# Optimization experiments

Hardware: AMD Instinct MI355X
Metric: run time of the kernel (lower is better)

The kernel has to match this reference:

```python
import jax, jax.numpy as jnp
import numpy as np

N, E = 50000, 800000
IN, HID, H, C = 128, 64, 4, 2
NEG_SLOPE = 0.2


def _gat_layer(h, src, dst, W, al, ar, b, out_dim, residual, resW=None, act='elu'):
    # h: [N, in]; W: [H*out, in]; al/ar: [H, out]; b: [H*out]
    n = h.shape[0]
    feat = (h @ W.T).reshape(n, H, out_dim)            # [N, H, out]
    el = jnp.einsum('nho,ho->nh', feat, al)            # [N, H]
    er = jnp.einsum('nho,ho->nh', feat, ar)            # [N, H]
    e = jax.nn.leaky_relu(el[src] + er[dst], NEG_SLOPE)  # [E, H]
    # segment softmax over incoming edges of each dst node
    emax = jax.ops.segment_max(e, dst, num_segments=n)
    ee = jnp.exp(e - emax[dst])
    denom = jax.ops.segment_sum(ee, dst, num_segments=n)
    alpha = ee / denom[dst]                             # [E, H]
    msg = feat[src] * alpha[:, :, None]                 # [E, H, out]
    rst = jax.ops.segment_sum(msg, dst, num_segments=n)  # [N, H, out]
    if residual == 'id':
        rst = rst + h.reshape(n, H, out_dim)
    elif residual == 'fc':
        rst = rst + (h @ resW.T).reshape(n, H, out_dim)
    rst = rst + b.reshape(1, H, out_dim)
    if act == 'elu':
        rst = jax.nn.elu(rst)
    else:  # softmax over last dim (F.softmax)
        rst = jax.nn.softmax(rst, axis=-1)
    return rst


def setup_inputs() -> dict:
    key = jax.random.key(0)
    ks = jax.random.split(key, 24)
    x = jax.random.normal(ks[0], (N, IN), dtype=jnp.float32)
    src = jax.random.randint(ks[1], (E,), 0, N)
    dst = jax.random.randint(ks[2], (E,), 0, N)
    s = 0.1
    d = {'x': x, 'src': src, 'dst': dst}
    # layer 1: IN -> (H, HID), no residual
    d['W1'] = jax.random.normal(ks[3], (H * HID, IN), dtype=jnp.float32) * s
    d['al1'] = jax.random.normal(ks[4], (H, HID), dtype=jnp.float32) * s
    d['ar1'] = jax.random.normal(ks[5], (H, HID), dtype=jnp.float32) * s
    d['b1'] = jnp.zeros((H * HID,), dtype=jnp.float32)
    # layers 2,3: H*HID -> (H, HID), identity residual
    d['W2'] = jax.random.normal(ks[6], (H * HID, H * HID), dtype=jnp.float32) * s
    d['al2'] = jax.random.normal(ks[7], (H, HID), dtype=jnp.float32) * s
    d['ar2'] = jax.random.normal(ks[8], (H, HID), dtype=jnp.float32) * s
    d['b2'] = jnp.zeros((H * HID,), dtype=jnp.float32)
    d['W3'] = jax.random.normal(ks[9], (H * HID, H * HID), dtype=jnp.float32) * s
    d['al3'] = jax.random.normal(ks[10], (H, HID), dtype=jnp.float32) * s
    d['ar3'] = jax.random.normal(ks[11], (H, HID), dtype=jnp.float32) * s
    d['b3'] = jnp.zeros((H * HID,), dtype=jnp.float32)
    # layer 4: H*HID -> (H, C), linear residual, softmax activation, mean over heads
    d['W4'] = jax.random.normal(ks[12], (H * C, H * HID), dtype=jnp.float32) * s
    d['al4'] = jax.random.normal(ks[13], (H, C), dtype=jnp.float32) * s
    d['ar4'] = jax.random.normal(ks[14], (H, C), dtype=jnp.float32) * s
    d['b4'] = jnp.zeros((H * C,), dtype=jnp.float32)
    d['resW4'] = jax.random.normal(ks[15], (H * C, H * HID), dtype=jnp.float32) * s
    return d


def reference(x, src, dst, W1, al1, ar1, b1, W2, al2, ar2, b2, W3, al3, ar3, b3, W4, al4, ar4, b4, resW4):
    h = _gat_layer(x, src, dst, W1, al1, ar1, b1, HID, 'none', act='elu').reshape(N, H * HID)
    h = _gat_layer(h, src, dst, W2, al2, ar2, b2, HID, 'id', act='elu').reshape(N, H * HID)
    h = _gat_layer(h, src, dst, W3, al3, ar3, b3, HID, 'id', act='elu').reshape(N, H * HID)
    h = _gat_layer(h, src, dst, W4, al4, ar4, b4, C, 'fc', resW=resW4, act='softmax')
    return h.mean(axis=1)  # [N, C]
```

## Files before the change

### kernel.cpp

```cpp
#include <hip/hip_runtime.h>
#include <hip/hip_bf16.h>
#include <math.h>


#define LEAKY_SLOPE 0.2f

typedef __bf16 bf16x8_t __attribute__((ext_vector_type(8)));
typedef float f32x4_t __attribute__((ext_vector_type(4)));

__device__ __forceinline__ float leaky(float x) { return x > 0.f ? x : LEAKY_SLOPE * x; }
__device__ __forceinline__ float eluf(float x)  { return x > 0.f ? x : expm1f(x); }
__device__ __forceinline__ float bflo(unsigned u) { return __uint_as_float(u << 16); }
__device__ __forceinline__ float bfhi(unsigned u) { return __uint_as_float(u & 0xffff0000u); }

__device__ __forceinline__ int rli(int v, int l) { return __builtin_amdgcn_readlane(v, l); }
__device__ __forceinline__ float rlf(float v, int l) {
  return __uint_as_float((unsigned)__builtin_amdgcn_readlane((int)__float_as_uint(v), l));
}
template <int CTRL>
__device__ __forceinline__ float dpp_add(float x) {
  int t = __builtin_amdgcn_update_dpp(0, (int)__float_as_uint(x), CTRL, 0xf, 0xf, false);
  return x + __uint_as_float((unsigned)t);
}
__device__ __forceinline__ float wsum_dpp(float x) {
  x = dpp_add<0x111>(x);
  x = dpp_add<0x112>(x);
  x = dpp_add<0x114>(x);
  x = dpp_add<0x118>(x);
  x = dpp_add<0x142>(x);
  x = dpp_add<0x143>(x);
  return rlf(x, 63);
}
__device__ __forceinline__ float wmax(float v) {
#pragma unroll
  for (int o = 32; o; o >>= 1) v = fmaxf(v, __shfl_xor(v, o));
  return v;
}
__device__ __forceinline__ float wsum_sh(float v) {
#pragma unroll
  for (int o = 32; o; o >>= 1) v += __shfl_xor(v, o);
  return v;
}

__global__ void hist_k(const int* __restrict__ dst, int* __restrict__ deg, int e) {
  int i = blockIdx.x * 256 + threadIdx.x;
  if (i < e) atomicAdd(&deg[dst[i]], 1);
}

__global__ __launch_bounds__(1024) void scan1_k(const int* __restrict__ deg,
                                                int* __restrict__ rowp,
                                                int* __restrict__ bsum, int n) {
  __shared__ int sd[1024];
  int tid = threadIdx.x;
  int i = blockIdx.x * 1024 + tid;
  int v = (i < n) ? deg[i] : 0;
  int x = v;
  sd[tid] = x;
  __syncthreads();
  for (int off = 1; off < 1024; off <<= 1) {
    int t = (tid >= off) ? sd[tid - off] : 0;
    __syncthreads();
    x += t;
    sd[tid] = x;
    __syncthreads();
  }
  if (i < n) rowp[i] = x - v;
  if (tid == 1023) bsum[blockIdx.x] = x;
}

__global__ __launch_bounds__(64) void scan2_k(int* __restrict__ bsum, int nb) {
  int lane = threadIdx.x;
  if (nb <= 64) {
    int v = (lane < nb) ? bsum[lane] : 0;
    int x = v;
#pragma unroll
    for (int off = 1; off < 64; off <<= 1) {
      int t = __shfl_up(x, off);
      if (lane >= off) x += t;
    }
    if (lane < nb) bsum[lane] = x - v;
    if (lane == 63) bsum[nb] = x;
  } else if (lane == 0) {
    int run = 0;
    for (int i = 0; i < nb; ++i) { int t = bsum[i]; bsum[i] = run; run += t; }
    bsum[nb] = run;
  }
}

__global__ void scan3_k(const int* __restrict__ bsum, int* __restrict__ rowp, int n, int nb) {
  int i = blockIdx.x * 256 + threadIdx.x;
  if (i < n) rowp[i] += bsum[i >> 10];
  if (i == n) rowp[n] = bsum[nb];
}

__global__ void scatter_k(const int* __restrict__ src, const int* __restrict__ dst,
                          const int* __restrict__ rowp, int* __restrict__ cur,
                          int* __restrict__ csrc, int e) {
  int i = blockIdx.x * 256 + threadIdx.x;
  if (i < e) {
    int d = dst[i];
    int p = atomicAdd(&cur[d], 1);
    csrc[rowp[d] + p] = src[i];
  }
}

__global__ void cvt_k(const float* __restrict__ a, __hip_bfloat16* __restrict__ b, int cnt) {
  int i = blockIdx.x * 256 + threadIdx.x;
  if (i < cnt) b[i] = __float2bfloat16(a[i]);
}

__global__ void cvtw_k(const float* __restrict__ W1, const float* __restrict__ W2,
                       const float* __restrict__ W3, const float* __restrict__ W4,
                       const float* __restrict__ rW4, __hip_bfloat16* __restrict__ W1b,
                       __hip_bfloat16* __restrict__ W2b, __hip_bfloat16* __restrict__ W3b,
                       __hip_bfloat16* __restrict__ Wcatb) {
  int i = blockIdx.x * 256 + threadIdx.x;
  if (i < 32768) W1b[i] = __float2bfloat16(W1[i]);
  else if (i < 98304)  { int j = i - 32768;  W2b[j] = __float2bfloat16(W2[j]); }
  else if (i < 163840) { int j = i - 98304;  W3b[j] = __float2bfloat16(W3[j]); }
  else if (i < 165888) { int j = i - 163840; Wcatb[j] = __float2bfloat16(W4[j]); }
  else if (i < 167936) { int j = i - 165888; Wcatb[2048 + j] = __float2bfloat16(rW4[j]); }
}

__global__ void wa_all_k(const float* __restrict__ W1, const float* __restrict__ al1,
                         const float* __restrict__ ar1, float* __restrict__ Wal1,
                         float* __restrict__ War1, const float* __restrict__ W2,
                         const float* __restrict__ al2, const float* __restrict__ ar2,
                         float* __restrict__ Wal2, float* __restrict__ War2,
                         const float* __restrict__ W3, const float* __restrict__ al3,
                         const float* __restrict__ ar3, float* __restrict__ Wal3,
                         float* __restrict__ War3) {
  int i = blockIdx.x * 256 + threadIdx.x;
  const float *W, *al, *ar;
  float *Wal, *War;
  int K, idx;
  if (i < 512)       { W = W1; al = al1; ar = ar1; Wal = Wal1; War = War1; K = 128; idx = i; }
  else if (i < 1536) { W = W2; al = al2; ar = ar2; Wal = Wal2; War = War2; K = 256; idx = i - 512; }
  else if (i < 2560) { W = W3; al = al3; ar = ar3; Wal = Wal3; War = War3; K = 256; idx = i - 1536; }
  else return;
  int hh = idx / K, col = idx - hh * K;
  float sl = 0.f, sr = 0.f;
  const float* wp = W + (size_t)(hh * 64) * K + col;
#pragma unroll 4
  for (int o = 0; o < 64; ++o) {
    float wv = wp[(size_t)o * K];
    sl = fmaf(al[hh * 64 + o], wv, sl);
    sr = fmaf(ar[hh * 64 + o], wv, sr);
  }
  Wal[idx] = sl;
  War[idx] = sr;
}

__global__ __launch_bounds__(256) void elproj_k(const float* __restrict__ x,
                                                const float* __restrict__ Wal,
                                                const float* __restrict__ War,
                                                float* __restrict__ el,
                                                float* __restrict__ er, int n) {
  int node = blockIdx.x * 4 + (threadIdx.x >> 6);
  int lane = threadIdx.x & 63;
  if (node >= n) return;
  float2 xv = *(const float2*)(x + (size_t)node * 128 + lane * 2);
#pragma unroll
  for (int hh = 0; hh < 4; ++hh) {
    float sl = xv.x * Wal[hh * 128 + 2 * lane] + xv.y * Wal[hh * 128 + 2 * lane + 1];
    float sr = xv.x * War[hh * 128 + 2 * lane] + xv.y * War[hh * 128 + 2 * lane + 1];
    sl = wsum_dpp(sl);
    sr = wsum_dpp(sr);
    if (lane == 0) {
      el[node * 4 + hh] = sl;
      er[node * 4 + hh] = sr;
    }
  }
}

template <int K>
__global__ __launch_bounds__(256) void gemm_mfma(const __hip_bfloat16* __restrict__ A,
                                                 const __hip_bfloat16* __restrict__ B,
                                                 __hip_bfloat16* __restrict__ featb, int n) {
  __shared__ __bf16 As[128 * 40];
  __shared__ __bf16 Bs[128 * 40];
  const int tid = threadIdx.x;
  const int lane = tid & 63, w = tid >> 6;
  const int tm = lane & 15, tq = lane >> 4;
  const int wm = (w & 1) * 64, wn = (w >> 1) * 64;
  const int r0 = blockIdx.x * 128, c0 = blockIdx.y * 128;
  const int srow = tid >> 1, sko = (tid & 1) * 16;

  f32x4_t acc[4][4];
#pragma unroll
  for (int i = 0; i < 4; ++i)
#pragma unroll
    for (int j = 0; j < 4; ++j) acc[i][j] = 0.f;

  for (int kk = 0; kk < K; kk += 32) {
    uint4 av0 = {0, 0, 0, 0}, av1 = {0, 0, 0, 0};
    int arw = r0 + srow;
    if (arw < n) {
      const uint4* p = (const uint4*)(A + (size_t)arw * K + kk + sko);
      av0 = p[0];
      av1 = p[1];
    }
    const uint4* q = (const uint4*)(B + (size_t)(c0 + srow) * K + kk + sko);
    uint4 bv0 = q[0], bv1 = q[1];
    __syncthreads();
    *(uint4*)&As[srow * 40 + sko] = av0;
    *(uint4*)&As[srow * 40 + sko + 8] = av1;
    *(uint4*)&Bs[srow * 40 + sko] = bv0;
    *(uint4*)&Bs[srow * 40 + sko + 8] = bv1;
    __syncthreads();
    bf16x8_t af[4], bfr[4];
#pragma unroll
    for (int i = 0; i < 4; ++i) af[i] = *(const bf16x8_t*)&As[(wm + i * 16 + tm) * 40 + tq * 8];
#pragma unroll
    for (int j = 0; j < 4; ++j) bfr[j] = *(const bf16x8_t*)&Bs[(wn + j * 16 + tm) * 40 + tq * 8];
#pragma unroll
    for (int i = 0; i < 4; ++i)
#pragma unroll
      for (int j = 0; j < 4; ++j)
        acc[i][j] = __builtin_amdgcn_mfma_f32_16x16x32_bf16(af[i], bfr[j], acc[i][j], 0, 0, 0);
  }

#pragma unroll
  for (int i = 0; i < 4; ++i) {
#pragma unroll
    for (int j = 0; j < 4; ++j) {
      int col = c0 + wn + j * 16 + tm;
      int hh = col >> 6, oo = col & 63;
#pragma unroll
      for (int rr = 0; rr < 4; ++rr) {
        int row = r0 + wm + i * 16 + tq * 4 + rr;
        if (row < n) featb[(size_t)row * 256 + oo * 4 + hh] = __float2bfloat16(acc[i][j][rr]);
      }
    }
  }
}

template <int RES, int NEXT>
__global__ __launch_bounds__(256) void agg64_k(const __hip_bfloat16* __restrict__ featb,
                                               const float* __restrict__ el,
                                               const float* __restrict__ er,
                                               const int* __restrict__ rowp,
                                               const int* __restrict__ csrc,
                                               const __hip_bfloat16* __restrict__ hinb,
                                               const float* __restrict__ bias,
                                               __hip_bfloat16* __restrict__ houtb,
                                               const float* __restrict__ Waln,
                                               const float* __restrict__ Warn,
                                               float* __restrict__ eln,
                                               float* __restrict__ ern, int n) {
  int node = blockIdx.x * 4 + (threadIdx.x >> 6);
  int lane = threadIdx.x & 63;
  if (node >= n) return;
  int s0 = rowp[node], s1 = rowp[node + 1];
  int deg = s1 - s0;
  float4 erv = *(const float4*)(er + (size_t)node * 4);
  float a0 = 0, a1 = 0, a2 = 0, a3 = 0;
  float i0 = 1.f, i1 = 1.f, i2 = 1.f, i3 = 1.f;

  if (deg <= 64) {
    int sown = 0;
    float x0 = 0.f, x1 = 0.f, x2 = 0.f, x3 = 0.f;
    if (lane < deg) {
      sown = csrc[s0 + lane];
      float4 e = *(const float4*)(el + (size_t)sown * 4);
      x0 = __expf(leaky(e.x + erv.x));
      x1 = __expf(leaky(e.y + erv.y));
      x2 = __expf(leaky(e.z + erv.z));
      x3 = __expf(leaky(e.w + erv.w));
    }
    float d0 = wsum_dpp(x0), d1 = wsum_dpp(x1), d2 = wsum_dpp(x2), d3 = wsum_dpp(x3);
    i0 = d0 > 0.f ? 1.f / d0 : 0.f;
    i1 = d1 > 0.f ? 1.f / d1 : 0.f;
    i2 = d2 > 0.f ? 1.f / d2 : 0.f;
    i3 = d3 > 0.f ? 1.f / d3 : 0.f;

    int k = 0;
    for (; k + 4 <= deg; k += 4) {
      int sk0 = rli(sown, k + 0), sk1 = rli(sown, k + 1);
      int sk2 = rli(sown, k + 2), sk3 = rli(sown, k + 3);
      uint2 u0 = ((const uint2*)(featb + ((size_t)sk0 << 8)))[lane];
      uint2 u1 = ((const uint2*)(featb + ((size_t)sk1 << 8)))[lane];
      uint2 u2 = ((const uint2*)(featb + ((size_t)sk2 << 8)))[lane];
      uint2 u3 = ((const uint2*)(featb + ((size_t)sk3 << 8)))[lane];
      float w00 = rlf(x0, k + 0), w10 = rlf(x1, k + 0), w20 = rlf(x2, k + 0), w30 = rlf(x3, k + 0);
      float w01 = rlf(x0, k + 1), w11 = rlf(x1, k + 1), w21 = rlf(x2, k + 1), w31 = rlf(x3, k + 1);
      float w02 = rlf(x0, k + 2), w12 = rlf(x1, k + 2), w22 = rlf(x2, k + 2), w32 = rlf(x3, k + 2);
      float w03 = rlf(x0, k + 3), w13 = rlf(x1, k + 3), w23 = rlf(x2, k + 3), w33 = rlf(x3, k + 3);
      a0 = fmaf(w00, bflo(u0.x), a0); a1 = fmaf(w10, bfhi(u0.x), a1);
      a2 = fmaf(w20, bflo(u0.y), a2); a3 = fmaf(w30, bfhi(u0.y), a3);
      a0 = fmaf(w01, bflo(u1.x), a0); a1 = fmaf(w11, bfhi(u1.x), a1);
      a2 = fmaf(w21, bflo(u1.y), a2); a3 = fmaf(w31, bfhi(u1.y), a3);
      a0 = fmaf(w02, bflo(u2.x), a0); a1 = fmaf(w12, bfhi(u2.x), a1);
      a2 = fmaf(w22, bflo(u2.y), a2); a3 = fmaf(w32, bfhi(u2.y), a3);
      a0 = fmaf(w03, bflo(u3.x), a0); a1 = fmaf(w13, bfhi(u3.x), a1);
      a2 = fmaf(w23, bflo(u3.y), a2); a3 = fmaf(w33, bfhi(u3.y), a3);
    }
    for (; k < deg; ++k) {
      int sk = rli(sown, k);
      float w0k = rlf(x0, k), w1k = rlf(x1, k), w2k = rlf(x2, k), w3k = rlf(x3, k);
      uint2 u = ((const uint2*)(featb + ((size_t)sk << 8)))[lane];
      a0 = fmaf(w0k, bflo(u.x), a0);
      a1 = fmaf(w1k, bfhi(u.x), a1);
      a2 = fmaf(w2k, bflo(u.y), a2);
      a3 = fmaf(w3k, bfhi(u.y), a3);
    }
  } else {
    float m0 = -INFINITY, m1 = -INFINITY, m2 = -INFINITY, m3 = -INFINITY;
    for (int k = s0 + lane; k < s1; k += 64) {
      int s = csrc[k];
      float4 e = *(const float4*)(el + (size_t)s * 4);
      m0 = fmaxf(m0, leaky(e.x + erv.x));
      m1 = fmaxf(m1, leaky(e.y + erv.y));
      m2 = fmaxf(m2, leaky(e.z + erv.z));
      m3 = fmaxf(m3, leaky(e.w + erv.w));
    }
    m0 = wmax(m0); m1 = wmax(m1); m2 = wmax(m2); m3 = wmax(m3);
    float d0 = 0, d1 = 0, d2 = 0, d3 = 0;
    for (int k = s0 + lane; k < s1; k += 64) {
      int s = csrc[k];
      float4 e = *(const float4*)(el + (size_t)s * 4);
      d0 += __expf(leaky(e.x + erv.x) - m0);
      d1 += __expf(leaky(e.y + erv.y) - m1);
      d2 += __expf(leaky(e.z + erv.z) - m2);
      d3 += __expf(leaky(e.w + erv.w) - m3);
    }
    d0 = wsum_sh(d0); d1 = wsum_sh(d1); d2 = wsum_sh(d2); d3 = wsum_sh(d3);
    float j0 = d0 > 0.f ? 1.f / d0 : 0.f;
    float j1 = d1 > 0.f ? 1.f / d1 : 0.f;
    float j2 = d2 > 0.f ? 1.f / d2 : 0.f;
    float j3 = d3 > 0.f ? 1.f / d3 : 0.f;
    for (int k = s0; k < s1; ++k) {
      int s = csrc[k];
      float4 e = *(const float4*)(el + (size_t)s * 4);
      float w0 = __expf(leaky(e.x + erv.x) - m0) * j0;
      float w1 = __expf(leaky(e.y + erv.y) - m1) * j1;
      float w2 = __expf(leaky(e.z + erv.z) - m2) * j2;
      float w3 = __expf(leaky(e.w + erv.w) - m3) * j3;
      uint2 u = ((const uint2*)(featb + ((size_t)s << 8)))[lane];
      a0 = fmaf(w0, bflo(u.x), a0);
      a1 = fmaf(w1, bfhi(u.x), a1);
      a2 = fmaf(w2, bflo(u.y), a2);
      a3 = fmaf(w3, bfhi(u.y), a3);
    }
  }

  size_t base = (size_t)node * 256;
  float v0 = a0 * i0 + bias[lane];
  float v1 = a1 * i1 + bias[64 + lane];
  float v2 = a2 * i2 + bias[128 + lane];
  float v3 = a3 * i3 + bias[192 + lane];
  if (RES) {
    v0 += __bfloat162float(hinb[base + lane]);
    v1 += __bfloat162float(hinb[base + 64 + lane]);
    v2 += __bfloat162float(hinb[base + 128 + lane]);
    v3 += __bfloat162float(hinb[base + 192 + lane]);
  }
  float o0 = eluf(v0), o1 = eluf(v1), o2 = eluf(v2), o3 = eluf(v3);
  houtb[base + lane]       = __float2bfloat16(o0);
  houtb[base + 64 + lane]  = __float2bfloat16(o1);
  houtb[base + 128 + lane] = __float2bfloat16(o2);
  houtb[base + 192 + lane] = __float2bfloat16(o3);
  if (NEXT) {
#pragma unroll
    for (int hh = 0; hh < 4; ++hh) {
      float sl = o0 * Waln[hh * 256 + lane] + o1 * Waln[hh * 256 + 64 + lane] +
                 o2 * Waln[hh * 256 + 128 + lane] + o3 * Waln[hh * 256 + 192 + lane];
      float sr = o0 * Warn[hh * 256 + lane] + o1 * Warn[hh * 256 + 64 + lane] +
                 o2 * Warn[hh * 256 + 128 + lane] + o3 * Warn[hh * 256 + 192 + lane];
      sl = wsum_dpp(sl);
      sr = wsum_dpp(sr);
      if (lane == 0) {
        eln[node * 4 + hh] = sl;
        ern[node * 4 + hh] = sr;
      }
    }
  }
}

__global__ __launch_bounds__(256) void l4mfma_k(const __hip_bfloat16* __restrict__ hb,
                                                const __hip_bfloat16* __restrict__ Wcat,
                                                float* __restrict__ feat4,
                                                float* __restrict__ res4, int n) {
  int wid = blockIdx.x * 4 + (threadIdx.x >> 6);
  int n16 = (n + 15) >> 4;
  if (wid >= n16) return;
  int lane = threadIdx.x & 63;
  int tm = lane & 15, tq = lane >> 4;
  int row = wid * 16 + tm;
  int rowc = row < n ? row : n - 1;
  const __hip_bfloat16* ap = hb + (size_t)rowc * 256 + tq * 8;
  const __hip_bfloat16* bp = Wcat + (size_t)tm * 256 + tq * 8;
  f32x4_t acc = {0.f, 0.f, 0.f, 0.f};
#pragma unroll
  for (int k = 0; k < 8; ++k) {
    bf16x8_t af = *(const bf16x8_t*)(ap + k * 32);
    bf16x8_t bf = *(const bf16x8_t*)(bp + k * 32);
    acc = __builtin_amdgcn_mfma_f32_16x16x32_bf16(af, bf, acc, 0, 0, 0);
  }
  float* dstp = (tm < 8) ? feat4 : res4;
  int cc = tm & 7;
#pragma unroll
  for (int r = 0; r < 4; ++r) {
    int node = wid * 16 + tq * 4 + r;
    if (node < n) dstp[(size_t)node * 8 + cc] = acc[r];
  }
}

__global__ void el4er4_k(const float* __restrict__ feat4, const float* __restrict__ al4,
                         const float* __restrict__ ar4, float* __restrict__ el4,
                         float* __restrict__ er4, int n) {
  int i = blockIdx.x * 256 + threadIdx.x;
  if (i >= n) return;
  float4 f0 = ((const float4*)(feat4 + (size_t)i * 8))[0];
  float4 f1 = ((const float4*)(feat4 + (size_t)i * 8))[1];
  float4 lv, rv;
  lv.x = f0.x * al4[0] + f0.y * al4[1];
  lv.y = f0.z * al4[2] + f0.w * al4[3];
  lv.z = f1.x * al4[4] + f1.y * al4[5];
  lv.w = f1.z * al4[6] + f1.w * al4[7];
  rv.x = f0.x * ar4[0] + f0.y * ar4[1];
  rv.y = f0.z * ar4[2] + f0.w * ar4[3];
  rv.z = f1.x * ar4[4] + f1.y * ar4[5];
  rv.w = f1.z * ar4[6] + f1.w * ar4[7];
  *(float4*)(el4 + (size_t)i * 4) = lv;
  *(float4*)(er4 + (size_t)i * 4) = rv;
}

__global__ __launch_bounds__(256) void agg4_k(const float* __restrict__ feat4,
                                              const float* __restrict__ el4,
                                              const float* __restrict__ er4,
                                              const int* __restrict__ rowp,
                                              const int* __restrict__ csrc,
                                              const float* __restrict__ res4,
                                              const float* __restrict__ b4,
                                              float* __restrict__ out, int n) {
  int node = blockIdx.x * 4 + (threadIdx.x >> 6);
  int lane = threadIdx.x & 63;
  if (node >= n) return;
  int s0 = rowp[node], s1 = rowp[node + 1];
  int deg = s1 - s0;
  float4 erv = *(const float4*)(er4 + (size_t)node * 4);
  float acc = 0.f;
  float scale = 1.f;
  int p = lane & 7, hh = p >> 1;

  if (deg <= 64) {
    int sown = 0;
    float x0 = 0.f, x1 = 0.f, x2 = 0.f, x3 = 0.f;
    if (lane < deg) {
      sown = csrc[s0 + lane];
      float4 e = *(const float4*)(el4 + (size_t)sown * 4);
      x0 = __expf(leaky(e.x + erv.x));
      x1 = __expf(leaky(e.y + erv.y));
      x2 = __expf(leaky(e.z + erv.z));
      x3 = __expf(leaky(e.w + erv.w));
    }
    float d0 = wsum_dpp(x0), d1 = wsum_dpp(x1), d2 = wsum_dpp(x2), d3 = wsum_dpp(x3);
    float i0 = d0 > 0.f ? 1.f / d0 : 0.f;
    float i1 = d1 > 0.f ? 1.f / d1 : 0.f;
    float i2 = d2 > 0.f ? 1.f / d2 : 0.f;
    float i3 = d3 > 0.f ? 1.f / d3 : 0.f;
    scale = (hh == 0) ? i0 : (hh == 1) ? i1 : (hh == 2) ? i2 : i3;
    int g = lane >> 3;
    int nt = (deg + 7) >> 3;
    for (int t = 0; t < nt; ++t) {
      int k = g + t * 8;
      bool ok = k < deg;
      int kk = k & 63;
      int sk = __shfl(sown, kk);
      float x0k = __shfl(x0, kk), x1k = __shfl(x1, kk);
      float x2k = __shfl(x2, kk), x3k = __shfl(x3, kk);
      float wk = (hh == 0) ? x0k : (hh == 1) ? x1k : (hh == 2) ? x2k : x3k;
      if (ok) acc = fmaf(wk, feat4[(size_t)sk * 8 + p], acc);
    }
    acc += __shfl_xor(acc, 8);
    acc += __shfl_xor(acc, 16);
    acc += __shfl_xor(acc, 32);
  } else {
    float m0 = -INFINITY, m1 = -INFINITY, m2 = -INFINITY, m3 = -INFINITY;
    for (int k = s0 + lane; k < s1; k += 64) {
      int s = csrc[k];
      float4 e = *(const float4*)(el4 + (size_t)s * 4);
      m0 = fmaxf(m0, leaky(e.x + erv.x));
      m1 = fmaxf(m1, leaky(e.y + erv.y));
      m2 = fmaxf(m2, leaky(e.z + erv.z));
      m3 = fmaxf(m3, leaky(e.w + erv.w));
    }
    m0 = wmax(m0); m1 = wmax(m1); m2 = wmax(m2); m3 = wmax(m3);
    float d0 = 0, d1 = 0, d2 = 0, d3 = 0;
    for (int k = s0 + lane; k < s1; k += 64) {
      int s = csrc[k];
      float4 e = *(const float4*)(el4 + (size_t)s * 4);
      d0 += __expf(leaky(e.x + erv.x) - m0);
      d1 += __expf(leaky(e.y + erv.y) - m1);
      d2 += __expf(leaky(e.z + erv.z) - m2);
      d3 += __expf(leaky(e.w + erv.w) - m3);
    }
    d0 = wsum_sh(d0); d1 = wsum_sh(d1); d2 = wsum_sh(d2); d3 = wsum_sh(d3);
    float i0 = d0 > 0.f ? 1.f / d0 : 0.f;
    float i1 = d1 > 0.f ? 1.f / d1 : 0.f;
    float i2 = d2 > 0.f ? 1.f / d2 : 0.f;
    float i3 = d3 > 0.f ? 1.f / d3 : 0.f;
    for (int k = s0; k < s1; ++k) {
      int s = csrc[k];
      float4 e = *(const float4*)(el4 + (size_t)s * 4);
      float w0 = __expf(leaky(e.x + erv.x) - m0) * i0;
      float w1 = __expf(leaky(e.y + erv.y) - m1) * i1;
      float w2 = __expf(leaky(e.z + erv.z) - m2) * i2;
      float w3 = __expf(leaky(e.w + erv.w) - m3) * i3;
      float wk = (hh == 0) ? w0 : (hh == 1) ? w1 : (hh == 2) ? w2 : w3;
      if (lane < 8) acc = fmaf(wk, feat4[(size_t)s * 8 + p], acc);
    }
  }

  float v = 0.f;
  if (lane < 8) v = acc * scale + res4[(size_t)node * 8 + lane] + b4[lane];
  float pv = __shfl_xor(v, 1);
  float mx = fmaxf(v, pv);
  float ex = __expf(v - mx);
  float sm = ex + __shfl_xor(ex, 1);
  float pr = ex / sm;
  float t = pr + __shfl_xor(pr, 2);
  t += __shfl_xor(t, 4);
  if (lane < 2) out[(size_t)node * 2 + lane] = t * 0.25f;
}

extern "C" void kernel_launch(void* const* d_in, const int* in_sizes, int n_in,
                              void* d_out, int out_size, void* d_ws, size_t ws_size,
                              hipStream_t stream) {
  const float* x   = (const float*)d_in[0];
  const int* src   = (const int*)d_in[1];
  const int* dst   = (const int*)d_in[2];
  const float* W1  = (const float*)d_in[3];
  const float* al1 = (const float*)d_in[4];
  const float* ar1 = (const float*)d_in[5];
  const float* b1  = (const float*)d_in[6];
  const float* W2  = (const float*)d_in[7];
  const float* al2 = (const float*)d_in[8];
  const float* ar2 = (const float*)d_in[9];
  const float* b2  = (const float*)d_in[10];
  const float* W3  = (const float*)d_in[11];
  const float* al3 = (const float*)d_in[12];
  const float* ar3 = (const float*)d_in[13];
  const float* b3  = (const float*)d_in[14];
  const float* W4  = (const float*)d_in[15];
  const float* al4 = (const float*)d_in[16];
  const float* ar4 = (const float*)d_in[17];
  const float* b4  = (const float*)d_in[18];
  const float* rW4 = (const float*)d_in[19];
  float* out = (float*)d_out;

  const int n = in_sizes[0] / 128;
  const int e = in_sizes[1];

  char* ws = (char*)d_ws;
  auto alloc = [&](size_t bytes) -> char* {
    char* p = ws;
    ws += (bytes + 255) & ~(size_t)255;
    return p;
  };
  __hip_bfloat16* featb = (__hip_bfloat16*)alloc((size_t)n * 256 * 2);
  __hip_bfloat16* h1b   = (__hip_bfloat16*)alloc((size_t)n * 256 * 2);
  __hip_bfloat16* h2b   = (__hip_bfloat16*)alloc((size_t)n * 256 * 2);
  __hip_bfloat16* h3b   = (__hip_bfloat16*)alloc((size_t)n * 256 * 2);
  __hip_bfloat16* xb    = (__hip_bfloat16*)alloc((size_t)n * 128 * 2);
  __hip_bfloat16* W1b   = (__hip_bfloat16*)alloc((size_t)256 * 128 * 2);
  __hip_bfloat16* W2b   = (__hip_bfloat16*)alloc((size_t)256 * 256 * 2);
  __hip_bfloat16* W3b   = (__hip_bfloat16*)alloc((size_t)256 * 256 * 2);
  __hip_bfloat16* Wcatb = (__hip_bfloat16*)alloc((size_t)16 * 256 * 2);
  float* Wal1 = (float*)alloc((size_t)4 * 128 * 4);
  float* War1 = (float*)alloc((size_t)4 * 128 * 4);
  float* Wal2 = (float*)alloc((size_t)4 * 256 * 4);
  float* War2 = (float*)alloc((size_t)4 * 256 * 4);
  float* Wal3 = (float*)alloc((size_t)4 * 256 * 4);
  float* War3 = (float*)alloc((size_t)4 * 256 * 4);
  float* elA   = (float*)alloc((size_t)n * 4 * 4);
  float* erA   = (float*)alloc((size_t)n * 4 * 4);
  float* elB   = (float*)alloc((size_t)n * 4 * 4);
  float* erB   = (float*)alloc((size_t)n * 4 * 4);
  float* feat4 = (float*)alloc((size_t)n * 8 * 4);
  float* res4  = (float*)alloc((size_t)n * 8 * 4);
  float* el4   = (float*)alloc((size_t)n * 4 * 4);
  float* er4   = (float*)alloc((size_t)n * 4 * 4);
  int* deg     = (int*)alloc((size_t)n * 4);
  int* cur     = (int*)alloc((size_t)n * 4);
  int* rowp    = (int*)alloc((size_t)(n + 1) * 4);
  int* csrc    = (int*)alloc((size_t)e * 4);
  int nb_scan  = (n + 1023) / 1024;
  int* bsum    = (int*)alloc((size_t)(nb_scan + 1) * 4);

  (void)hipMemsetAsync(deg, 0, (size_t)n * 4, stream);
  (void)hipMemsetAsync(cur, 0, (size_t)n * 4, stream);
  hist_k<<<(e + 255) / 256, 256, 0, stream>>>(dst, deg, e);
  scan1_k<<<nb_scan, 1024, 0, stream>>>(deg, rowp, bsum, n);
  scan2_k<<<1, 64, 0, stream>>>(bsum, nb_scan);
  scan3_k<<<(n + 256) / 256, 256, 0, stream>>>(bsum, rowp, n, nb_scan);
  scatter_k<<<(e + 255) / 256, 256, 0, stream>>>(src, dst, rowp, cur, csrc, e);

  cvt_k<<<(n * 128 + 255) / 256, 256, 0, stream>>>(x, xb, n * 128);
  cvtw_k<<<(167936 + 255) / 256, 256, 0, stream>>>(W1, W2, W3, W4, rW4, W1b, W2b, W3b, Wcatb);
  wa_all_k<<<(2560 + 255) / 256, 256, 0, stream>>>(W1, al1, ar1, Wal1, War1,
                                                   W2, al2, ar2, Wal2, War2,
                                                   W3, al3, ar3, Wal3, War3);

  dim3 ggrid((n + 127) / 128, 2);
  int nb4 = (n + 3) / 4;

  elproj_k<<<nb4, 256, 0, stream>>>(x, Wal1, War1, elA, erA, n);
  gemm_mfma<128><<<ggrid, 256, 0, stream>>>(xb, W1b, featb, n);
  agg64_k<0, 1><<<nb4, 256, 0, stream>>>(featb, elA, erA, rowp, csrc, nullptr, b1, h1b,
                                         Wal2, War2, elB, erB, n);
  gemm_mfma<256><<<ggrid, 256, 0, stream>>>(h1b, W2b, featb, n);
  agg64_k<1, 1><<<nb4, 256, 0, stream>>>(featb, elB, erB, rowp, csrc, h1b, b2, h2b,
                                         Wal3, War3, elA, erA, n);
  gemm_mfma<256><<<ggrid, 256, 0, stream>>>(h2b, W3b, featb, n);
  agg64_k<1, 0><<<nb4, 256, 0, stream>>>(featb, elA, erA, rowp, csrc, h2b, b3, h3b,
                                         nullptr, nullptr, nullptr, nullptr, n);
  int n16 = (n + 15) / 16;
  l4mfma_k<<<(n16 + 3) / 4, 256, 0, stream>>>(h3b, Wcatb, feat4, res4, n);
  el4er4_k<<<(n + 255) / 256, 256, 0, stream>>>(feat4, al4, ar4, el4, er4, n);
  agg4_k<<<nb4, 256, 0, stream>>>(feat4, el4, er4, rowp, csrc, res4, b4, out, n);
}
```

Baseline: 541.7 us.

## Fuse attention logit projection into GEMM epilogue and stage edge weights in LDS

Computes el/er directly from the MFMA accumulators in the GEMM epilogue with lane shuffles. This removes the precomputed W·a vectors, the elproj kernel and the next-layer projection tail in the aggregation kernel. The x and weight bf16 conversions merge into one launch, and the layer-4 el/er computation is folded into l4mfma. In the aggregation kernels, per-edge weights and source indices are staged in shared memory instead of being fetched with readlane/shfl. The trade-offs are more epilogue shuffles in the GEMM, extra LDS traffic in the aggregation loops, and el/er now computed from fp32 accumulators rather than from fp32 inputs.

```diff
diff --git a/kernel.cpp b/kernel.cpp
--- a/kernel.cpp
+++ b/kernel.cpp
@@ -104,79 +104,30 @@
   }
 }
 
-__global__ void cvt_k(const float* __restrict__ a, __hip_bfloat16* __restrict__ b, int cnt) {
+__global__ void cvtall_k(const float* __restrict__ x, const float* __restrict__ W1,
+                         const float* __restrict__ W2, const float* __restrict__ W3,
+                         const float* __restrict__ W4, const float* __restrict__ rW4,
+                         __hip_bfloat16* __restrict__ xb, __hip_bfloat16* __restrict__ W1b,
+                         __hip_bfloat16* __restrict__ W2b, __hip_bfloat16* __restrict__ W3b,
+                         __hip_bfloat16* __restrict__ Wcatb, int nx) {
   int i = blockIdx.x * 256 + threadIdx.x;
-  if (i < cnt) b[i] = __float2bfloat16(a[i]);
-}
-
-__global__ void cvtw_k(const float* __restrict__ W1, const float* __restrict__ W2,
-                       const float* __restrict__ W3, const float* __restrict__ W4,
-                       const float* __restrict__ rW4, __hip_bfloat16* __restrict__ W1b,
-                       __hip_bfloat16* __restrict__ W2b, __hip_bfloat16* __restrict__ W3b,
-                       __hip_bfloat16* __restrict__ Wcatb) {
-  int i = blockIdx.x * 256 + threadIdx.x;
-  if (i < 32768) W1b[i] = __float2bfloat16(W1[i]);
-  else if (i < 98304)  { int j = i - 32768;  W2b[j] = __float2bfloat16(W2[j]); }
-  else if (i < 163840) { int j = i - 98304;  W3b[j] = __float2bfloat16(W3[j]); }
-  else if (i < 165888) { int j = i - 163840; Wcatb[j] = __float2bfloat16(W4[j]); }
-  else if (i < 167936) { int j = i - 165888; Wcatb[2048 + j] = __float2bfloat16(rW4[j]); }
-}
-
-__global__ void wa_all_k(const float* __restrict__ W1, const float* __restrict__ al1,
-                         const float* __restrict__ ar1, float* __restrict__ Wal1,
-                         float* __restrict__ War1, const float* __restrict__ W2,
-                         const float* __restrict__ al2, const float* __restrict__ ar2,
-                         float* __restrict__ Wal2, float* __restrict__ War2,
-                         const float* __restrict__ W3, const float* __restrict__ al3,
-                         const float* __restrict__ ar3, float* __restrict__ Wal3,
-                         float* __restrict__ War3) {
-  int i = blockIdx.x * 256 + threadIdx.x;
-  const float *W, *al, *ar;
-  float *Wal, *War;
-  int K, idx;
-  if (i < 512)       { W = W1; al = al1; ar = ar1; Wal = Wal1; War = War1; K = 128; idx = i; }
-  else if (i < 1536) { W = W2; al = al2; ar = ar2; Wal = Wal2; War = War2; K = 256; idx = i - 512; }
-  else if (i < 2560) { W = W3; al = al3; ar = ar3; Wal = Wal3; War = War3; K = 256; idx = i - 1536; }
-  else return;
-  int hh = idx / K, col = idx - hh * K;
-  float sl = 0.f, sr = 0.f;
-  const float* wp = W + (size_t)(hh * 64) * K + col;
-#pragma unroll 4
-  for (int o = 0; o < 64; ++o) {
-    float wv = wp[(size_t)o * K];
-    sl = fmaf(al[hh * 64 + o], wv, sl);
-    sr = fmaf(ar[hh * 64 + o], wv, sr);
-  }
-  Wal[idx] = sl;
-  War[idx] = sr;
-}
-
-__global__ __launch_bounds__(256) void elproj_k(const float* __restrict__ x,
-                                                const float* __restrict__ Wal,
-                                                const float* __restrict__ War,
-                                                float* __restrict__ el,
-                                                float* __restrict__ er, int n) {
-  int node = blockIdx.x * 4 + (threadIdx.x >> 6);
-  int lane = threadIdx.x & 63;
-  if (node >= n) return;
-  float2 xv = *(const float2*)(x + (size_t)node * 128 + lane * 2);
-#pragma unroll
-  for (int hh = 0; hh < 4; ++hh) {
-    float sl = xv.x * Wal[hh * 128 + 2 * lane] + xv.y * Wal[hh * 128 + 2 * lane + 1];
-    float sr = xv.x * War[hh * 128 + 2 * lane] + xv.y * War[hh * 128 + 2 * lane + 1];
-    sl = wsum_dpp(sl);
-    sr = wsum_dpp(sr);
-    if (lane == 0) {
-      el[node * 4 + hh] = sl;
-      er[node * 4 + hh] = sr;
-    }
-  }
+  if (i < nx) { xb[i] = __float2bfloat16(x[i]); return; }
+  int j = i - nx;
+  if (j < 32768) W1b[j] = __float2bfloat16(W1[j]);
+  else if (j < 98304)  { int k = j - 32768;  W2b[k] = __float2bfloat16(W2[k]); }
+  else if (j < 163840) { int k = j - 98304;  W3b[k] = __float2bfloat16(W3[k]); }
+  else if (j < 165888) { int k = j - 163840; Wcatb[k] = __float2bfloat16(W4[k]); }
+  else if (j < 167936) { int k = j - 165888; Wcatb[2048 + k] = __float2bfloat16(rW4[k]); }
 }
 
 template <int K>
 __global__ __launch_bounds__(256) void gemm_mfma(const __hip_bfloat16* __restrict__ A,
                                                  const __hip_bfloat16* __restrict__ B,
-                                                 __hip_bfloat16* __restrict__ featb, int n) {
+                                                 __hip_bfloat16* __restrict__ featb,
+                                                 const float* __restrict__ al,
+                                                 const float* __restrict__ ar,
+                                                 float* __restrict__ el,
+                                                 float* __restrict__ er, int n) {
   __shared__ __bf16 As[128 * 40];
   __shared__ __bf16 Bs[128 * 40];
   const int tid = threadIdx.x;
@@ -233,9 +184,41 @@
       }
     }
   }
-}
-
-template <int RES, int NEXT>
+
+  {
+    const int hd = (c0 + wn) >> 6;
+    float alv[4], arv[4];
+#pragma unroll
+    for (int j = 0; j < 4; ++j) {
+      alv[j] = al[hd * 64 + j * 16 + tm];
+      arv[j] = ar[hd * 64 + j * 16 + tm];
+    }
+#pragma unroll
+    for (int i = 0; i < 4; ++i) {
+#pragma unroll
+      for (int rr = 0; rr < 4; ++rr) {
+        float se = acc[i][0][rr] * alv[0] + acc[i][1][rr] * alv[1] +
+                   acc[i][2][rr] * alv[2] + acc[i][3][rr] * alv[3];
+        float sr2 = acc[i][0][rr] * arv[0] + acc[i][1][rr] * arv[1] +
+                    acc[i][2][rr] * arv[2] + acc[i][3][rr] * arv[3];
+#pragma unroll
+        for (int o = 1; o < 16; o <<= 1) {
+          se += __shfl_xor(se, o);
+          sr2 += __shfl_xor(sr2, o);
+        }
+        if (tm == 0) {
+          int row = r0 + wm + i * 16 + tq * 4 + rr;
+          if (row < n) {
+            el[(size_t)row * 4 + hd] = se;
+            er[(size_t)row * 4 + hd] = sr2;
+          }
+        }
+      }
+    }
+  }
+}
+
+template <int RES>
 __global__ __launch_bounds__(256) void agg64_k(const __hip_bfloat16* __restrict__ featb,
                                                const float* __restrict__ el,
                                                const float* __restrict__ er,
@@ -243,12 +226,10 @@
                                                const int* __restrict__ csrc,
                                                const __hip_bfloat16* __restrict__ hinb,
                                                const float* __restrict__ bias,
-                                               __hip_bfloat16* __restrict__ houtb,
-                                               const float* __restrict__ Waln,
-                                               const float* __restrict__ Warn,
-                                               float* __restrict__ eln,
-                                               float* __restrict__ ern, int n) {
-  int node = blockIdx.x * 4 + (threadIdx.x >> 6);
+                                               __hip_bfloat16* __restrict__ houtb, int n) {
+  __shared__ float wsh[4][256];
+  int wv = threadIdx.x >> 6;
+  int node = blockIdx.x * 4 + wv;
   int lane = threadIdx.x & 63;
   if (node >= n) return;
   int s0 = rowp[node], s1 = rowp[node + 1];
@@ -274,6 +255,9 @@
     i2 = d2 > 0.f ? 1.f / d2 : 0.f;
     i3 = d3 > 0.f ? 1.f / d3 : 0.f;
 
+    float4 wq = {x0, x1, x2, x3};
+    *(float4*)&wsh[wv][lane * 4] = wq;
+
     int k = 0;
     for (; k + 4 <= deg; k += 4) {
       int sk0 = rli(sown, k + 0), sk1 = rli(sown, k + 1);
@@ -282,27 +266,27 @@
       uint2 u1 = ((const uint2*)(featb + ((size_t)sk1 << 8)))[lane];
       uint2 u2 = ((const uint2*)(featb + ((size_t)sk2 << 8)))[lane];
       uint2 u3 = ((const uint2*)(featb + ((size_t)sk3 << 8)))[lane];
-      float w00 = rlf(x0, k + 0), w10 = rlf(x1, k + 0), w20 = rlf(x2, k + 0), w30 = rlf(x3, k + 0);
-      float w01 = rlf(x0, k + 1), w11 = rlf(x1, k + 1), w21 = rlf(x2, k + 1), w31 = rlf(x3, k + 1);
-      float w02 = rlf(x0, k + 2), w12 = rlf(x1, k + 2), w22 = rlf(x2, k + 2), w32 = rlf(x3, k + 2);
-      float w03 = rlf(x0, k + 3), w13 = rlf(x1, k + 3), w23 = rlf(x2, k + 3), w33 = rlf(x3, k + 3);
-      a0 = fmaf(w00, bflo(u0.x), a0); a1 = fmaf(w10, bfhi(u0.x), a1);
-      a2 = fmaf(w20, bflo(u0.y), a2); a3 = fmaf(w30, bfhi(u0.y), a3);
-      a0 = fmaf(w01, bflo(u1.x), a0); a1 = fmaf(w11, bfhi(u1.x), a1);
-      a2 = fmaf(w21, bflo(u1.y), a2); a3 = fmaf(w31, bfhi(u1.y), a3);
-      a0 = fmaf(w02, bflo(u2.x), a0); a1 = fmaf(w12, bfhi(u2.x), a1);
-      a2 = fmaf(w22, bflo(u2.y), a2); a3 = fmaf(w32, bfhi(u2.y), a3);
-      a0 = fmaf(w03, bflo(u3.x), a0); a1 = fmaf(w13, bfhi(u3.x), a1);
-      a2 = fmaf(w23, bflo(u3.y), a2); a3 = fmaf(w33, bfhi(u3.y), a3);
+      float4 w0 = *(const float4*)&wsh[wv][(k + 0) * 4];
+      float4 w1 = *(const float4*)&wsh[wv][(k + 1) * 4];
+      float4 w2 = *(const float4*)&wsh[wv][(k + 2) * 4];
+      float4 w3 = *(const float4*)&wsh[wv][(k + 3) * 4];
+      a0 = fmaf(w0.x, bflo(u0.x), a0); a1 = fmaf(w0.y, bfhi(u0.x), a1);
+      a2 = fmaf(w0.z, bflo(u0.y), a2); a3 = fmaf(w0.w, bfhi(u0.y), a3);
+      a0 = fmaf(w1.x, bflo(u1.x), a0); a1 = fmaf(w1.y, bfhi(u1.x), a1);
+      a2 = fmaf(w1.z, bflo(u1.y), a2); a3 = fmaf(w1.w, bfhi(u1.y), a3);
+      a0 = fmaf(w2.x, bflo(u2.x), a0); a1 = fmaf(w2.y, bfhi(u2.x), a1);
+      a2 = fmaf(w2.z, bflo(u2.y), a2); a3 = fmaf(w2.w, bfhi(u2.y), a3);
+      a0 = fmaf(w3.x, bflo(u3.x), a0); a1 = fmaf(w3.y, bfhi(u3.x), a1);
+      a2 = fmaf(w3.z, bflo(u3.y), a2); a3 = fmaf(w3.w, bfhi(u3.y), a3);
     }
     for (; k < deg; ++k) {
       int sk = rli(sown, k);
-      float w0k = rlf(x0, k), w1k = rlf(x1, k), w2k = rlf(x2, k), w3k = rlf(x3, k);
       uint2 u = ((const uint2*)(featb + ((size_t)sk << 8)))[lane];
-      a0 = fmaf(w0k, bflo(u.x), a0);
-      a1 = fmaf(w1k, bfhi(u.x), a1);
-      a2 = fmaf(w2k, bflo(u.y), a2);
-      a3 = fmaf(w3k, bfhi(u.y), a3);
+      float4 wk = *(const float4*)&wsh[wv][k * 4];
+      a0 = fmaf(wk.x, bflo(u.x), a0);
+      a1 = fmaf(wk.y, bfhi(u.x), a1);
+      a2 = fmaf(wk.z, bflo(u.y), a2);
+      a3 = fmaf(wk.w, bfhi(u.y), a3);
     }
   } else {
     float m0 = -INFINITY, m1 = -INFINITY, m2 = -INFINITY, m3 = -INFINITY;
@@ -355,32 +339,20 @@
     v2 += __bfloat162float(hinb[base + 128 + lane]);
     v3 += __bfloat162float(hinb[base + 192 + lane]);
   }
-  float o0 = eluf(v0), o1 = eluf(v1), o2 = eluf(v2), o3 = eluf(v3);
-  houtb[base + lane]       = __float2bfloat16(o0);
-  houtb[base + 64 + lane]  = __float2bfloat16(o1);
-  houtb[base + 128 + lane] = __float2bfloat16(o2);
-  houtb[base + 192 + lane] = __float2bfloat16(o3);
-  if (NEXT) {
-#pragma unroll
-    for (int hh = 0; hh < 4; ++hh) {
-      float sl = o0 * Waln[hh * 256 + lane] + o1 * Waln[hh * 256 + 64 + lane] +
-                 o2 * Waln[hh * 256 + 128 + lane] + o3 * Waln[hh * 256 + 192 + lane];
-      float sr = o0 * Warn[hh * 256 + lane] + o1 * Warn[hh * 256 + 64 + lane] +
-                 o2 * Warn[hh * 256 + 128 + lane] + o3 * Warn[hh * 256 + 192 + lane];
-      sl = wsum_dpp(sl);
-      sr = wsum_dpp(sr);
-      if (lane == 0) {
-        eln[node * 4 + hh] = sl;
-        ern[node * 4 + hh] = sr;
-      }
-    }
-  }
+  houtb[base + lane]       = __float2bfloat16(eluf(v0));
+  houtb[base + 64 + lane]  = __float2bfloat16(eluf(v1));
+  houtb[base + 128 + lane] = __float2bfloat16(eluf(v2));
+  houtb[base + 192 + lane] = __float2bfloat16(eluf(v3));
 }
 
 __global__ __launch_bounds__(256) void l4mfma_k(const __hip_bfloat16* __restrict__ hb,
                                                 const __hip_bfloat16* __restrict__ Wcat,
+                                                const float* __restrict__ al4,
+                                                const float* __restrict__ ar4,
                                                 float* __restrict__ feat4,
-                                                float* __restrict__ res4, int n) {
+                                                float* __restrict__ res4,
+                                                float* __restrict__ el4,
+                                                float* __restrict__ er4, int n) {
   int wid = blockIdx.x * 4 + (threadIdx.x >> 6);
   int n16 = (n + 15) >> 4;
   if (wid >= n16) return;
@@ -399,31 +371,23 @@
   }
   float* dstp = (tm < 8) ? feat4 : res4;
   int cc = tm & 7;
+  float a4 = (tm < 8) ? al4[tm] : 0.f;
+  float r4 = (tm < 8) ? ar4[tm] : 0.f;
 #pragma unroll
   for (int r = 0; r < 4; ++r) {
     int node = wid * 16 + tq * 4 + r;
-    if (node < n) dstp[(size_t)node * 8 + cc] = acc[r];
-  }
-}
-
-__global__ void el4er4_k(const float* __restrict__ feat4, const float* __restrict__ al4,
-                         const float* __restrict__ ar4, float* __restrict__ el4,
-                         float* __restrict__ er4, int n) {
-  int i = blockIdx.x * 256 + threadIdx.x;
-  if (i >= n) return;
-  float4 f0 = ((const float4*)(feat4 + (size_t)i * 8))[0];
-  float4 f1 = ((const float4*)(feat4 + (size_t)i * 8))[1];
-  float4 lv, rv;
-  lv.x = f0.x * al4[0] + f0.y * al4[1];
-  lv.y = f0.z * al4[2] + f0.w * al4[3];
-  lv.z = f1.x * al4[4] + f1.y * al4[5];
-  lv.w = f1.z * al4[6] + f1.w * al4[7];
-  rv.x = f0.x * ar4[0] + f0.y * ar4[1];
-  rv.y = f0.z * ar4[2] + f0.w * ar4[3];
-  rv.z = f1.x * ar4[4] + f1.y * ar4[5];
-  rv.w = f1.z * ar4[6] + f1.w * ar4[7];
-  *(float4*)(el4 + (size_t)i * 4) = lv;
-  *(float4*)(er4 + (size_t)i * 4) = rv;
+    float te = acc[r] * a4;
+    float tr = acc[r] * r4;
+    te += __shfl_xor(te, 1);
+    tr += __shfl_xor(tr, 1);
+    if (node < n) {
+      dstp[(size_t)node * 8 + cc] = acc[r];
+      if (tm < 8 && (tm & 1) == 0) {
+        el4[(size_t)node * 4 + (tm >> 1)] = te;
+        er4[(size_t)node * 4 + (tm >> 1)] = tr;
+      }
+    }
+  }
 }
 
 __global__ __launch_bounds__(256) void agg4_k(const float* __restrict__ feat4,
@@ -434,7 +398,10 @@
                                               const float* __restrict__ res4,
                                               const float* __restrict__ b4,
                                               float* __restrict__ out, int n) {
-  int node = blockIdx.x * 4 + (threadIdx.x >> 6);
+  __shared__ int ssh[4][64];
+  __shared__ float wsh[4][256];
+  int wv = threadIdx.x >> 6;
+  int node = blockIdx.x * 4 + wv;
   int lane = threadIdx.x & 63;
   if (node >= n) return;
   int s0 = rowp[node], s1 = rowp[node + 1];
@@ -461,16 +428,17 @@
     float i2 = d2 > 0.f ? 1.f / d2 : 0.f;
     float i3 = d3 > 0.f ? 1.f / d3 : 0.f;
     scale = (hh == 0) ? i0 : (hh == 1) ? i1 : (hh == 2) ? i2 : i3;
+    ssh[wv][lane] = sown;
+    float4 wq = {x0, x1, x2, x3};
+    *(float4*)&wsh[wv][lane * 4] = wq;
     int g = lane >> 3;
     int nt = (deg + 7) >> 3;
     for (int t = 0; t < nt; ++t) {
       int k = g + t * 8;
       bool ok = k < deg;
       int kk = k & 63;
-      int sk = __shfl(sown, kk);
-      float x0k = __shfl(x0, kk), x1k = __shfl(x1, kk);
-      float x2k = __shfl(x2, kk), x3k = __shfl(x3, kk);
-      float wk = (hh == 0) ? x0k : (hh == 1) ? x1k : (hh == 2) ? x2k : x3k;
+      int sk = ssh[wv][kk];
+      float wk = wsh[wv][kk * 4 + hh];
       if (ok) acc = fmaf(wk, feat4[(size_t)sk * 8 + p], acc);
     }
     acc += __shfl_xor(acc, 8);
@@ -568,16 +536,8 @@
   __hip_bfloat16* W2b   = (__hip_bfloat16*)alloc((size_t)256 * 256 * 2);
   __hip_bfloat16* W3b   = (__hip_bfloat16*)alloc((size_t)256 * 256 * 2);
   __hip_bfloat16* Wcatb = (__hip_bfloat16*)alloc((size_t)16 * 256 * 2);
-  float* Wal1 = (float*)alloc((size_t)4 * 128 * 4);
-  float* War1 = (float*)alloc((size_t)4 * 128 * 4);
-  float* Wal2 = (float*)alloc((size_t)4 * 256 * 4);
-  float* War2 = (float*)alloc((size_t)4 * 256 * 4);
-  float* Wal3 = (float*)alloc((size_t)4 * 256 * 4);
-  float* War3 = (float*)alloc((size_t)4 * 256 * 4);
-  float* elA   = (float*)alloc((size_t)n * 4 * 4);
-  float* erA   = (float*)alloc((size_t)n * 4 * 4);
-  float* elB   = (float*)alloc((size_t)n * 4 * 4);
-  float* erB   = (float*)alloc((size_t)n * 4 * 4);
+  float* el    = (float*)alloc((size_t)n * 4 * 4);
+  float* er    = (float*)alloc((size_t)n * 4 * 4);
   float* feat4 = (float*)alloc((size_t)n * 8 * 4);
   float* res4  = (float*)alloc((size_t)n * 8 * 4);
   float* el4   = (float*)alloc((size_t)n * 4 * 4);
@@ -597,27 +557,20 @@
   scan3_k<<<(n + 256) / 256, 256, 0, stream>>>(bsum, rowp, n, nb_scan);
   scatter_k<<<(e + 255) / 256, 256, 0, stream>>>(src, dst, rowp, cur, csrc, e);
 
-  cvt_k<<<(n * 128 + 255) / 256, 256, 0, stream>>>(x, xb, n * 128);
-  cvtw_k<<<(167936 + 255) / 256, 256, 0, stream>>>(W1, W2, W3, W4, rW4, W1b, W2b, W3b, Wcatb);
-  wa_all_k<<<(2560 + 255) / 256, 256, 0, stream>>>(W1, al1, ar1, Wal1, War1,
-                                                   W2, al2, ar2, Wal2, War2,
-                                                   W3, al3, ar3, Wal3, War3);
+  int nx = n * 128;
+  cvtall_k<<<(nx + 167936 + 255) / 256, 256, 0, stream>>>(x, W1, W2, W3, W4, rW4, xb, W1b,
+                                                          W2b, W3b, Wcatb, nx);
 
   dim3 ggrid((n + 127) / 128, 2);
   int nb4 = (n + 3) / 4;
 
-  elproj_k<<<nb4, 256, 0, stream>>>(x, Wal1, War1, elA, erA, n);
-  gemm_mfma<128><<<ggrid, 256, 0, stream>>>(xb, W1b, featb, n);
-  agg64_k<0, 1><<<nb4, 256, 0, stream>>>(featb, elA, erA, rowp, csrc, nullptr, b1, h1b,
-                                         Wal2, War2, elB, erB, n);
-  gemm_mfma<256><<<ggrid, 256, 0, stream>>>(h1b, W2b, featb, n);
-  agg64_k<1, 1><<<nb4, 256, 0, stream>>>(featb, elB, erB, rowp, csrc, h1b, b2, h2b,
-                                         Wal3, War3, elA, erA, n);
-  gemm_mfma<256><<<ggrid, 256, 0, stream>>>(h2b, W3b, featb, n);
-  agg64_k<1, 0><<<nb4, 256, 0, stream>>>(featb, elA, erA, rowp, csrc, h2b, b3, h3b,
-                                         nullptr, nullptr, nullptr, nullptr, n);
+  gemm_mfma<128><<<ggrid, 256, 0, stream>>>(xb, W1b, featb, al1, ar1, el, er, n);
+  agg64_k<0><<<nb4, 256, 0, stream>>>(featb, el, er, rowp, csrc, nullptr, b1, h1b, n);
+  gemm_mfma<256><<<ggrid, 256, 0, stream>>>(h1b, W2b, featb, al2, ar2, el, er, n);
+  agg64_k<1><<<nb4, 256, 0, stream>>>(featb, el, er, rowp, csrc, h1b, b2, h2b, n);
+  gemm_mfma<256><<<ggrid, 256, 0, stream>>>(h2b, W3b, featb, al3, ar3, el, er, n);
+  agg64_k<1><<<nb4, 256, 0, stream>>>(featb, el, er, rowp, csrc, h2b, b3, h3b, n);
   int n16 = (n + 15) / 16;
-  l4mfma_k<<<(n16 + 3) / 4, 256, 0, stream>>>(h3b, Wcatb, feat4, res4, n);
-  el4er4_k<<<(n + 255) / 256, 256, 0, stream>>>(feat4, al4, ar4, el4, er4, n);
+  l4mfma_k<<<(n16 + 3) / 4, 256, 0, stream>>>(h3b, Wcatb, al4, ar4, feat4, res4, el4, er4, n);
   agg4_k<<<nb4, 256, 0, stream>>>(feat4, el4, er4, rowp, csrc, res4, b4, out, n);
 }
```

Result: faster. 515.7 us (-4.8%).
